# Kernel tuning notes

Hardware: AMD Instinct MI355X
Metric: run time of the kernel (lower is better)

The kernel has to match this reference:

```python
import jax, jax.numpy as jnp
import numpy as np

T, B, K = 512, 512, 128  # seq_length, batch_size, num_tags


def setup_inputs() -> dict:
    key = jax.random.key(0)
    k1, k2, k3, k4, k5 = jax.random.split(key, 5)
    emissions = jax.random.normal(k1, (T, B, K), dtype=jnp.float32)
    tags = jax.random.randint(k2, (T, B), 0, K, dtype=jnp.int32)
    mask = jnp.ones((T, B), dtype=jnp.int32)
    start_transitions = jax.random.uniform(k3, (K,), jnp.float32, -0.1, 0.1)
    end_transitions = jax.random.uniform(k4, (K,), jnp.float32, -0.1, 0.1)
    transitions = jax.random.uniform(k5, (K, K), jnp.float32, -0.1, 0.1)
    return {
        "emissions": emissions,
        "tags": tags,
        "mask": mask,
        "start_transitions": start_transitions,
        "end_transitions": end_transitions,
        "transitions": transitions,
    }


def reference(emissions, tags, mask, start_transitions, end_transitions, transitions):
    # emissions: [T,B,K], tags/mask: [T,B]; reduction='sum' (negative is the loss in practice)
    Tn, Bn, Kn = emissions.shape
    maskf = mask.astype(emissions.dtype)
    b_idx = jnp.arange(Bn)

    # ---- numerator: score of the given tag path (fully vectorized) ----
    em_tag = jnp.take_along_axis(emissions, tags[:, :, None], axis=2)[:, :, 0]  # [T,B]
    numerator = start_transitions[tags[0]] + em_tag[0]
    trans_path = transitions[tags[:-1], tags[1:]]  # [T-1,B]
    numerator = numerator + jnp.sum((trans_path + em_tag[1:]) * maskf[1:], axis=0)
    seq_ends = mask.astype(jnp.int32).sum(axis=0) - 1  # [B]
    last_tags = tags[seq_ends, b_idx]
    numerator = numerator + end_transitions[last_tags]

    # ---- denominator: forward algorithm (log-partition) via scan ----
    alpha0 = start_transitions + emissions[0]  # [B,K]

    def step(alpha, xs):
        em_i, m_i = xs  # [B,K], [B]
        # [B,K_prev,K_next] broadcast-add, logsumexp over previous tag
        nxt = jax.nn.logsumexp(alpha[:, :, None] + transitions[None, :, :] + em_i[:, None, :], axis=1)
        alpha = jnp.where(m_i[:, None], nxt, alpha)
        return alpha, None

    alpha, _ = jax.lax.scan(step, alpha0, (emissions[1:], mask[1:].astype(bool)))
    denominator = jax.nn.logsumexp(alpha + end_transitions, axis=1)  # [B]

    llh = numerator - denominator
    return jnp.sum(llh)  # reduction='sum'
```

## Files before the change

### kernel.cpp

```cpp
#include <hip/hip_runtime.h>
#include <hip/hip_bf16.h>

#define Tn 512
#define Bn 512
#define Kn 128

typedef __bf16 bf16_t;
typedef __bf16 bf16x8 __attribute__((ext_vector_type(8)));
typedef float f32x4 __attribute__((ext_vector_type(4)));
typedef unsigned int u32;
typedef u32 u32x2 __attribute__((ext_vector_type(2)));
typedef u32 u32x4 __attribute__((ext_vector_type(4)));

#define NEXPEM 4096

__device__ __forceinline__ u32 pack2bf(float a, float b) {
    bf16_t ha = (bf16_t)a, hb = (bf16_t)b;
    u32 ua = (u32)__builtin_bit_cast(unsigned short, ha);
    u32 ub = (u32)__builtin_bit_cast(unsigned short, hb);
    return ua | (ub << 16);
}

template<int PRE>
__global__ __launch_bounds__(256)
void crf_pre(const float* __restrict__ em, const int* __restrict__ tags,
             const int* __restrict__ mask, const float* __restrict__ startT,
             const float* __restrict__ endT, const float* __restrict__ trans,
             u32* __restrict__ X, bf16_t* __restrict__ frags,
             float* __restrict__ num, float* __restrict__ out)
{
    const int bid = blockIdx.x;
    const int tid = threadIdx.x;

    if (bid < NEXPEM) {
        if (!PRE) return;
        const size_t N = (size_t)Tn * Bn * Kn;
        const size_t nth = (size_t)NEXPEM * 256;
        for (size_t base = ((size_t)bid * 256 + tid) * 8; base < N; base += nth * 8) {
            const f32x4 a = *reinterpret_cast<const f32x4*>(em + base);
            const f32x4 b = *reinterpret_cast<const f32x4*>(em + base + 4);
            u32x4 w;
            w[0] = pack2bf(__expf(a[0]), __expf(a[1]));
            w[1] = pack2bf(__expf(a[2]), __expf(a[3]));
            w[2] = pack2bf(__expf(b[0]), __expf(b[1]));
            w[3] = pack2bf(__expf(b[2]), __expf(b[3]));
            *reinterpret_cast<u32x4*>(X + base / 2) = w;
        }
        return;
    }

    const int b = bid - NEXPEM;
    if (b == Bn) {
        if (tid == 0) out[0] = 0.f;
        for (int idx = tid; idx < 2*8*4*64*8; idx += blockDim.x) {
            const int e   = idx & 7;
            const int l   = (idx >> 3) & 63;
            const int ks  = (idx >> 9) & 3;
            const int m   = (idx >> 11) & 7;
            const int dir = (idx >> 14) & 1;
            const int c = l & 15, g = l >> 4;
            const int k = 32*ks + 8*g + e;
            const int j = 32*(m >> 1) + 4*(m & 1) + 8*(c >> 2) + (c & 3);
            const float v = (dir == 0) ? trans[k*Kn + j] : trans[j*Kn + k];
            frags[idx] = (bf16_t)__expf(v);
        }
        return;
    }

    float s = 0.f;
    int cnt = 0;
    for (int t = tid; t < Tn; t += 256) {
        const int mk = mask[t*Bn + b];
        cnt += (mk != 0);
        if (t >= 1 && mk != 0) {
            const int tp = tags[(t-1)*Bn + b];
            const int tc = tags[t*Bn + b];
            s += trans[tp*Kn + tc] + em[(size_t)t*Bn*Kn + (size_t)b*Kn + tc];
        }
    }
    __shared__ float sred[256];
    __shared__ int   cred[256];
    sred[tid] = s; cred[tid] = cnt;
    __syncthreads();
    for (int off = 128; off > 0; off >>= 1) {
        if (tid < off) { sred[tid] += sred[tid+off]; cred[tid] += cred[tid+off]; }
        __syncthreads();
    }
    if (tid == 0) {
        const int t0tag = tags[b];
        const float n0 = startT[t0tag] + em[(size_t)b*Kn + t0tag];
        int seq_end = cred[0] - 1;
        if (seq_end < 0) seq_end = 0;
        const int lastTag = tags[seq_end*Bn + b];
        num[b] = n0 + sred[0] + endT[lastTag];
    }
}

template<int PRE>
__global__ __launch_bounds__(512, 1)
void crf_main(const float* __restrict__ em, const u32* __restrict__ Xp,
              const int* __restrict__ maskp,
              const float* __restrict__ startT, const float* __restrict__ endT,
              const bf16_t* __restrict__ frags,
              float* __restrict__ vws, float* __restrict__ Cws)
{
    const int bid = blockIdx.x;
    const int dir = bid & 1;
    const int b0  = (bid >> 1) * 16;
    const int tid = threadIdx.x;
    const int mw  = tid >> 6;
    const int l   = tid & 63;
    const int c = l & 15, g = l >> 4;
    const int batch = b0 + c;
    const int ksw  = mw >> 1, half = mw & 1;
    const int bj   = 32*ksw + 4*half;

    __shared__ __align__(16) u32x4 exchg[2][4][64];

    bf16x8 af[4];
    {
        const bf16_t* fb = frags + (size_t)dir * 16384;
        #pragma unroll
        for (int ks = 0; ks < 4; ++ks)
            af[ks] = *reinterpret_cast<const bf16x8*>(fb + ((mw*4 + ks)*64 + l)*8);
    }

    f32x4 up;
    u32 ownprev0, ownprev1;
    float Cacc = 0.f;
    {
        const float* sv = dir ? endT : startT;
        const int t0 = dir ? 511 : 0;
        const f32x4 e4 = *reinterpret_cast<const f32x4*>(
            em + ((size_t)t0*Bn + batch)*Kn + bj + 8*g);
        const float* s4p = sv + bj + 8*g;
        f32x4 y;
        #pragma unroll
        for (int r = 0; r < 4; ++r) {
            const float s = s4p[r];
            y[r]  = __expf(s + e4[r]);
            up[r] = __expf(s);
        }
        ownprev0 = pack2bf(y[0], y[1]);
        ownprev1 = pack2bf(y[2], y[3]);
        u32* slot = reinterpret_cast<u32*>(&exchg[1][ksw][l]) + 2*half;
        u32x2 nw2 = {ownprev0, ownprev1};
        *reinterpret_cast<u32x2*>(slot) = nw2;
    }

    const int M = 256 - dir;

    const u32 laneX = (u32)(((batch*Kn) + bj + 8*g) >> 1);
    const u32 laneE = (u32)((batch*Kn) + bj + 8*g);
    const u32 laneM = (u32)batch;
    const long stepX = dir ? -(long)(Bn*Kn)   : (long)(Bn*Kn);
    const long stepE = dir ? -(long)(2*Bn*Kn) : (long)(2*Bn*Kn);
    const long stepM = dir ? -(long)(2*Bn)    : (long)(2*Bn);
    long uXA, uXB, uEA, uEB, uMA, uMB;
    {
        const int tA  = dir ? 510 : 1, tB  = dir ? 509 : 2;
        const int tmA = dir ? 511 : 1, tmB = dir ? 510 : 2;
        uXA = (long)tA * (Bn*Kn/2);  uXB = (long)tB * (Bn*Kn/2);
        uEA = (long)tA * (Bn*Kn);    uEB = (long)tB * (Bn*Kn);
        uMA = (long)tmA * Bn;        uMB = (long)tmB * Bn;
    }

    u32x2 xA, xB; f32x4 eA, eB; int mkA, mkB;
    auto load_tile = [&](u32x2& xd, f32x4& ed, int& mk, long& uX, long& uE, long& uM) {
        if (PRE) { xd = *reinterpret_cast<const u32x2*>(Xp + uX + laneX); uX += stepX; }
        else     { ed = *reinterpret_cast<const f32x4*>(em + uE + laneE); uE += stepE; }
        mk = maskp[uM + laneM]; uM += stepM;
    };

    auto iter = [&](u32x2& xcur, f32x4& ecur, int& mkcur,
                    long& uX, long& uE, long& uM, bool rs, int par) {
        asm volatile("s_waitcnt lgkmcnt(0)" ::: "memory");
        __builtin_amdgcn_s_barrier();
        __builtin_amdgcn_sched_barrier(0);

        const u32x4 bs0 = exchg[par][0][l];
        const u32x4 bs1 = exchg[par][1][l];
        const u32x4 bs2 = exchg[par][2][l];
        const u32x4 bs3 = exchg[par][3][l];

        f32x4 a0 = {0.f, 0.f, 0.f, 0.f}, a1 = {0.f, 0.f, 0.f, 0.f};
        a0 = __builtin_amdgcn_mfma_f32_16x16x32_bf16(af[0], __builtin_bit_cast(bf16x8, bs0), a0, 0, 0, 0);
        a1 = __builtin_amdgcn_mfma_f32_16x16x32_bf16(af[2], __builtin_bit_cast(bf16x8, bs2), a1, 0, 0, 0);
        a0 = __builtin_amdgcn_mfma_f32_16x16x32_bf16(af[1], __builtin_bit_cast(bf16x8, bs1), a0, 0, 0, 0);
        a1 = __builtin_amdgcn_mfma_f32_16x16x32_bf16(af[3], __builtin_bit_cast(bf16x8, bs3), a1, 0, 0, 0);
        const f32x4 acc = a0 + a1;

        const bool mk = (mkcur != 0);
        float sc = 1.f, klog = 0.f;
        if (rs) {
            int ex = (int)((bs0[0] >> 7) & 0xFF) - 127;
            ex = __shfl(ex, c, 64);
            sc = __uint_as_float((u32)((127 - ex) & 0xFF) << 23);
            klog = (float)ex * 0.6931471805599453f;
        }

        f32x4 xf;
        if (PRE) {
            xf[0] = __uint_as_float(xcur[0] << 16);
            xf[1] = __uint_as_float(xcur[0] & 0xffff0000u);
            xf[2] = __uint_as_float(xcur[1] << 16);
            xf[3] = __uint_as_float(xcur[1] & 0xffff0000u);
        } else {
            #pragma unroll
            for (int r = 0; r < 4; ++r) xf[r] = __expf(ecur[r]);
        }

        u32 nw0, nw1;
        if (dir == 0) {
            f32x4 y;
            #pragma unroll
            for (int r = 0; r < 4; ++r) {
                float a = acc[r];
                if (rs) a *= sc;
                y[r] = a * xf[r];
            }
            nw0 = pack2bf(y[0], y[1]);
            nw1 = pack2bf(y[2], y[3]);
            nw0 = mk ? nw0 : ownprev0;
            nw1 = mk ? nw1 : ownprev1;
            ownprev0 = nw0; ownprev1 = nw1;
            if (rs && mk) Cacc += klog;
        } else {
            f32x4 y;
            #pragma unroll
            for (int r = 0; r < 4; ++r) {
                float un = mk ? acc[r] : up[r];
                if (rs) un *= sc;
                up[r] = un;
                y[r] = un * xf[r];
            }
            nw0 = pack2bf(y[0], y[1]);
            nw1 = pack2bf(y[2], y[3]);
            if (rs) Cacc += klog;
        }

        u32* slot = reinterpret_cast<u32*>(&exchg[par ^ 1][ksw][l]) + 2*half;
        u32x2 nw2 = {nw0, nw1};
        *reinterpret_cast<u32x2*>(slot) = nw2;

        load_tile(xcur, ecur, mkcur, uX, uE, uM);
        __builtin_amdgcn_sched_barrier(0xF);
    };

    load_tile(xA, eA, mkA, uXA, uEA, uMA);
    load_tile(xB, eB, mkB, uXB, uEB, uMB);
    __builtin_amdgcn_sched_barrier(0xF);

    int m = 1;
    for (; m + 3 <= M; m += 4) {
        iter(xA, eA, mkA, uXA, uEA, uMA, false, 1);
        iter(xB, eB, mkB, uXB, uEB, uMB, false, 0);
        iter(xA, eA, mkA, uXA, uEA, uMA, false, 1);
        iter(xB, eB, mkB, uXB, uEB, uMB, true,  0);
    }
    for (; m <= M; ++m) {
        if (m & 1) iter(xA, eA, mkA, uXA, uEA, uMA, false, 1);
        else       iter(xB, eB, mkB, uXB, uEB, uMB, false, 0);
    }

    float* vrow = vws + ((size_t)(dir*Bn + batch))*Kn + bj + 8*g;
    f32x4 fv;
    if (dir) {
        fv = up;
    } else {
        fv[0] = __uint_as_float(ownprev0 << 16);
        fv[1] = __uint_as_float(ownprev0 & 0xffff0000u);
        fv[2] = __uint_as_float(ownprev1 << 16);
        fv[3] = __uint_as_float(ownprev1 & 0xffff0000u);
    }
    *reinterpret_cast<f32x4*>(vrow) = fv;
    if (mw == 0 && g == 0) Cws[dir*Bn + batch] = Cacc;
}

__global__ void crf_combine(const float* __restrict__ vws, const float* __restrict__ Cws,
                            const float* __restrict__ num, float* __restrict__ out)
{
    const int b = blockIdx.x;
    const int tid = threadIdx.x;
    const float p = vws[(size_t)b*Kn + tid] * vws[(size_t)(Bn + b)*Kn + tid];
    __shared__ float red[128];
    red[tid] = p;
    __syncthreads();
    for (int off = 64; off > 0; off >>= 1) {
        if (tid < off) red[tid] += red[tid + off];
        __syncthreads();
    }
    if (tid == 0) {
        const float den = Cws[b] + Cws[Bn + b] + logf(red[0]);
        atomicAdd(out, num[b] - den);
    }
}

extern "C" void kernel_launch(void* const* d_in, const int* in_sizes, int n_in,
                              void* d_out, int out_size, void* d_ws, size_t ws_size,
                              hipStream_t stream)
{
    const float* em     = (const float*)d_in[0];
    const int*   tags   = (const int*)d_in[1];
    const int*   mask   = (const int*)d_in[2];
    const float* startT = (const float*)d_in[3];
    const float* endT   = (const float*)d_in[4];
    const float* trans  = (const float*)d_in[5];

    const size_t XBYTES = (size_t)Tn * Bn * Kn * 2;
    const size_t SMALL  = 65536 + 2048 + 4096 + 524288;
    const bool pre = (ws_size >= XBYTES + SMALL);

    char* ws = (char*)d_ws;
    u32*  X  = (u32*)ws;
    char* base = pre ? (ws + XBYTES) : ws;
    bf16_t* frags = (bf16_t*)base;
    float*  num   = (float*)(base + 65536);
    float*  Cws   = (float*)(base + 65536 + 2048);
    float*  vws   = (float*)(base + 65536 + 2048 + 4096);
    float*  out   = (float*)d_out;

    if (pre) {
        hipLaunchKernelGGL((crf_pre<1>), dim3(NEXPEM + Bn + 1), dim3(256), 0, stream,
                           em, tags, mask, startT, endT, trans, X, frags, num, out);
        hipLaunchKernelGGL((crf_main<1>), dim3(64), dim3(512), 0, stream,
                           em, X, mask, startT, endT, frags, vws, Cws);
    } else {
        hipLaunchKernelGGL((crf_pre<0>), dim3(NEXPEM + Bn + 1), dim3(256), 0, stream,
                           em, tags, mask, startT, endT, trans, X, frags, num, out);
        hipLaunchKernelGGL((crf_main<0>), dim3(64), dim3(512), 0, stream,
                           em, X, mask, startT, endT, frags, vws, Cws);
    }
    hipLaunchKernelGGL(crf_combine, dim3(Bn), dim3(128), 0, stream,
                       vws, Cws, num, out);
}
```

Before: 142.9 us.

## Drop bf16 exp-emission precompute pass and compute exp inline in scan

Removes the separate pass that exponentiated the whole emission tensor into a bf16 workspace copy. The recurrent main kernel now loads fp32 emissions directly and applies exp per step. This avoids a full read-plus-write sweep over the large tensor before the scan, but doubles the bytes the latency-sensitive scan loads per step and adds exp work there. The numerator is also reworked into time-chunked per-batch partial sums that the combine kernel finishes, and the transition-fragment setup now spreads one element per thread across many blocks.

```diff
diff --git a/kernel.cpp b/kernel.cpp
--- a/kernel.cpp
+++ b/kernel.cpp
@@ -4,6 +4,7 @@
 #define Tn 512
 #define Bn 512
 #define Kn 128
+#define NUMCH 16
 
 typedef __bf16 bf16_t;
 typedef __bf16 bf16x8 __attribute__((ext_vector_type(8)));
@@ -12,8 +13,6 @@
 typedef u32 u32x2 __attribute__((ext_vector_type(2)));
 typedef u32 u32x4 __attribute__((ext_vector_type(4)));
 
-#define NEXPEM 4096
-
 __device__ __forceinline__ u32 pack2bf(float a, float b) {
     bf16_t ha = (bf16_t)a, hb = (bf16_t)b;
     u32 ua = (u32)__builtin_bit_cast(unsigned short, ha);
@@ -21,85 +20,54 @@
     return ua | (ub << 16);
 }
 
-template<int PRE>
 __global__ __launch_bounds__(256)
 void crf_pre(const float* __restrict__ em, const int* __restrict__ tags,
-             const int* __restrict__ mask, const float* __restrict__ startT,
-             const float* __restrict__ endT, const float* __restrict__ trans,
-             u32* __restrict__ X, bf16_t* __restrict__ frags,
-             float* __restrict__ num, float* __restrict__ out)
+             const int* __restrict__ mask, const float* __restrict__ trans,
+             bf16_t* __restrict__ frags, float* __restrict__ numpart,
+             int* __restrict__ cntpart, float* __restrict__ out)
 {
     const int bid = blockIdx.x;
     const int tid = threadIdx.x;
 
-    if (bid < NEXPEM) {
-        if (!PRE) return;
-        const size_t N = (size_t)Tn * Bn * Kn;
-        const size_t nth = (size_t)NEXPEM * 256;
-        for (size_t base = ((size_t)bid * 256 + tid) * 8; base < N; base += nth * 8) {
-            const f32x4 a = *reinterpret_cast<const f32x4*>(em + base);
-            const f32x4 b = *reinterpret_cast<const f32x4*>(em + base + 4);
-            u32x4 w;
-            w[0] = pack2bf(__expf(a[0]), __expf(a[1]));
-            w[1] = pack2bf(__expf(a[2]), __expf(a[3]));
-            w[2] = pack2bf(__expf(b[0]), __expf(b[1]));
-            w[3] = pack2bf(__expf(b[2]), __expf(b[3]));
-            *reinterpret_cast<u32x4*>(X + base / 2) = w;
-        }
+    if (bid < 2*NUMCH) {
+        const int ch = bid >> 1, bh = bid & 1;
+        const int b  = bh*256 + tid;
+        const int t0 = ch * (Tn / NUMCH);
+        float s = 0.f;
+        int cnt = 0;
+        int tagprev = (t0 > 0) ? tags[(t0-1)*Bn + b] : 0;
+        for (int t = t0; t < t0 + Tn/NUMCH; ++t) {
+            const int mk = mask[t*Bn + b];
+            const int tagcur = tags[t*Bn + b];
+            if (mk != 0) {
+                cnt++;
+                if (t >= 1)
+                    s += trans[tagprev*Kn + tagcur]
+                       + em[(size_t)t*Bn*Kn + (size_t)b*Kn + tagcur];
+            }
+            tagprev = tagcur;
+        }
+        numpart[ch*Bn + b] = s;
+        cntpart[ch*Bn + b] = cnt;
         return;
     }
 
-    const int b = bid - NEXPEM;
-    if (b == Bn) {
-        if (tid == 0) out[0] = 0.f;
-        for (int idx = tid; idx < 2*8*4*64*8; idx += blockDim.x) {
-            const int e   = idx & 7;
-            const int l   = (idx >> 3) & 63;
-            const int ks  = (idx >> 9) & 3;
-            const int m   = (idx >> 11) & 7;
-            const int dir = (idx >> 14) & 1;
-            const int c = l & 15, g = l >> 4;
-            const int k = 32*ks + 8*g + e;
-            const int j = 32*(m >> 1) + 4*(m & 1) + 8*(c >> 2) + (c & 3);
-            const float v = (dir == 0) ? trans[k*Kn + j] : trans[j*Kn + k];
-            frags[idx] = (bf16_t)__expf(v);
-        }
-        return;
-    }
-
-    float s = 0.f;
-    int cnt = 0;
-    for (int t = tid; t < Tn; t += 256) {
-        const int mk = mask[t*Bn + b];
-        cnt += (mk != 0);
-        if (t >= 1 && mk != 0) {
-            const int tp = tags[(t-1)*Bn + b];
-            const int tc = tags[t*Bn + b];
-            s += trans[tp*Kn + tc] + em[(size_t)t*Bn*Kn + (size_t)b*Kn + tc];
-        }
-    }
-    __shared__ float sred[256];
-    __shared__ int   cred[256];
-    sred[tid] = s; cred[tid] = cnt;
-    __syncthreads();
-    for (int off = 128; off > 0; off >>= 1) {
-        if (tid < off) { sred[tid] += sred[tid+off]; cred[tid] += cred[tid+off]; }
-        __syncthreads();
-    }
-    if (tid == 0) {
-        const int t0tag = tags[b];
-        const float n0 = startT[t0tag] + em[(size_t)b*Kn + t0tag];
-        int seq_end = cred[0] - 1;
-        if (seq_end < 0) seq_end = 0;
-        const int lastTag = tags[seq_end*Bn + b];
-        num[b] = n0 + sred[0] + endT[lastTag];
-    }
-}
-
-template<int PRE>
+    if (bid == 2*NUMCH && tid == 0) out[0] = 0.f;
+    const int idx = (bid - 2*NUMCH)*256 + tid;
+    const int e   = idx & 7;
+    const int l   = (idx >> 3) & 63;
+    const int ks  = (idx >> 9) & 3;
+    const int m   = (idx >> 11) & 7;
+    const int dir = (idx >> 14) & 1;
+    const int c = l & 15, g = l >> 4;
+    const int k = 32*ks + 8*g + e;
+    const int j = 32*(m >> 1) + 4*(m & 1) + 8*(c >> 2) + (c & 3);
+    const float v = (dir == 0) ? trans[k*Kn + j] : trans[j*Kn + k];
+    frags[idx] = (bf16_t)__expf(v);
+}
+
 __global__ __launch_bounds__(512, 1)
-void crf_main(const float* __restrict__ em, const u32* __restrict__ Xp,
-              const int* __restrict__ maskp,
+void crf_main(const float* __restrict__ em, const int* __restrict__ maskp,
               const float* __restrict__ startT, const float* __restrict__ endT,
               const bf16_t* __restrict__ frags,
               float* __restrict__ vws, float* __restrict__ Cws)
@@ -150,30 +118,25 @@
 
     const int M = 256 - dir;
 
-    const u32 laneX = (u32)(((batch*Kn) + bj + 8*g) >> 1);
     const u32 laneE = (u32)((batch*Kn) + bj + 8*g);
     const u32 laneM = (u32)batch;
-    const long stepX = dir ? -(long)(Bn*Kn)   : (long)(Bn*Kn);
     const long stepE = dir ? -(long)(2*Bn*Kn) : (long)(2*Bn*Kn);
     const long stepM = dir ? -(long)(2*Bn)    : (long)(2*Bn);
-    long uXA, uXB, uEA, uEB, uMA, uMB;
+    long uEA, uEB, uMA, uMB;
     {
         const int tA  = dir ? 510 : 1, tB  = dir ? 509 : 2;
         const int tmA = dir ? 511 : 1, tmB = dir ? 510 : 2;
-        uXA = (long)tA * (Bn*Kn/2);  uXB = (long)tB * (Bn*Kn/2);
         uEA = (long)tA * (Bn*Kn);    uEB = (long)tB * (Bn*Kn);
         uMA = (long)tmA * Bn;        uMB = (long)tmB * Bn;
     }
 
-    u32x2 xA, xB; f32x4 eA, eB; int mkA, mkB;
-    auto load_tile = [&](u32x2& xd, f32x4& ed, int& mk, long& uX, long& uE, long& uM) {
-        if (PRE) { xd = *reinterpret_cast<const u32x2*>(Xp + uX + laneX); uX += stepX; }
-        else     { ed = *reinterpret_cast<const f32x4*>(em + uE + laneE); uE += stepE; }
+    f32x4 eA, eB; int mkA, mkB;
+    auto load_tile = [&](f32x4& ed, int& mk, long& uE, long& uM) {
+        ed = *reinterpret_cast<const f32x4*>(em + uE + laneE); uE += stepE;
         mk = maskp[uM + laneM]; uM += stepM;
     };
 
-    auto iter = [&](u32x2& xcur, f32x4& ecur, int& mkcur,
-                    long& uX, long& uE, long& uM, bool rs, int par) {
+    auto iter = [&](f32x4& ecur, int& mkcur, long& uE, long& uM, bool rs, int par) {
         asm volatile("s_waitcnt lgkmcnt(0)" ::: "memory");
         __builtin_amdgcn_s_barrier();
         __builtin_amdgcn_sched_barrier(0);
@@ -200,15 +163,8 @@
         }
 
         f32x4 xf;
-        if (PRE) {
-            xf[0] = __uint_as_float(xcur[0] << 16);
-            xf[1] = __uint_as_float(xcur[0] & 0xffff0000u);
-            xf[2] = __uint_as_float(xcur[1] << 16);
-            xf[3] = __uint_as_float(xcur[1] & 0xffff0000u);
-        } else {
-            #pragma unroll
-            for (int r = 0; r < 4; ++r) xf[r] = __expf(ecur[r]);
-        }
+        #pragma unroll
+        for (int r = 0; r < 4; ++r) xf[r] = __expf(ecur[r]);
 
         u32 nw0, nw1;
         if (dir == 0) {
@@ -243,24 +199,24 @@
         u32x2 nw2 = {nw0, nw1};
         *reinterpret_cast<u32x2*>(slot) = nw2;
 
-        load_tile(xcur, ecur, mkcur, uX, uE, uM);
+        load_tile(ecur, mkcur, uE, uM);
         __builtin_amdgcn_sched_barrier(0xF);
     };
 
-    load_tile(xA, eA, mkA, uXA, uEA, uMA);
-    load_tile(xB, eB, mkB, uXB, uEB, uMB);
+    load_tile(eA, mkA, uEA, uMA);
+    load_tile(eB, mkB, uEB, uMB);
     __builtin_amdgcn_sched_barrier(0xF);
 
     int m = 1;
     for (; m + 3 <= M; m += 4) {
-        iter(xA, eA, mkA, uXA, uEA, uMA, false, 1);
-        iter(xB, eB, mkB, uXB, uEB, uMB, false, 0);
-        iter(xA, eA, mkA, uXA, uEA, uMA, false, 1);
-        iter(xB, eB, mkB, uXB, uEB, uMB, true,  0);
+        iter(eA, mkA, uEA, uMA, false, 1);
+        iter(eB, mkB, uEB, uMB, false, 0);
+        iter(eA, mkA, uEA, uMA, false, 1);
+        iter(eB, mkB, uEB, uMB, true,  0);
     }
     for (; m <= M; ++m) {
-        if (m & 1) iter(xA, eA, mkA, uXA, uEA, uMA, false, 1);
-        else       iter(xB, eB, mkB, uXB, uEB, uMB, false, 0);
+        if (m & 1) iter(eA, mkA, uEA, uMA, false, 1);
+        else       iter(eB, mkB, uEB, uMB, false, 0);
     }
 
     float* vrow = vws + ((size_t)(dir*Bn + batch))*Kn + bj + 8*g;
@@ -278,21 +234,35 @@
 }
 
 __global__ void crf_combine(const float* __restrict__ vws, const float* __restrict__ Cws,
-                            const float* __restrict__ num, float* __restrict__ out)
+                            const float* __restrict__ numpart, const int* __restrict__ cntpart,
+                            const int* __restrict__ tags, const float* __restrict__ em,
+                            const float* __restrict__ startT, const float* __restrict__ endT,
+                            float* __restrict__ out)
 {
     const int b = blockIdx.x;
     const int tid = threadIdx.x;
     const float p = vws[(size_t)b*Kn + tid] * vws[(size_t)(Bn + b)*Kn + tid];
     __shared__ float red[128];
+    __shared__ float sp[NUMCH];
+    __shared__ int   cp[NUMCH];
     red[tid] = p;
+    if (tid < NUMCH) { sp[tid] = numpart[tid*Bn + b]; cp[tid] = cntpart[tid*Bn + b]; }
     __syncthreads();
     for (int off = 64; off > 0; off >>= 1) {
         if (tid < off) red[tid] += red[tid + off];
         __syncthreads();
     }
     if (tid == 0) {
+        float s = 0.f; int cnt = 0;
+        #pragma unroll
+        for (int ch = 0; ch < NUMCH; ++ch) { s += sp[ch]; cnt += cp[ch]; }
+        const int t0tag = tags[b];
+        int seq_end = cnt - 1;
+        if (seq_end < 0) seq_end = 0;
+        const int lastTag = tags[seq_end*Bn + b];
+        const float num = startT[t0tag] + em[(size_t)b*Kn + t0tag] + s + endT[lastTag];
         const float den = Cws[b] + Cws[Bn + b] + logf(red[0]);
-        atomicAdd(out, num[b] - den);
+        atomicAdd(out, num - den);
     }
 }
 
@@ -307,30 +277,18 @@
     const float* endT   = (const float*)d_in[4];
     const float* trans  = (const float*)d_in[5];
 
-    const size_t XBYTES = (size_t)Tn * Bn * Kn * 2;
-    const size_t SMALL  = 65536 + 2048 + 4096 + 524288;
-    const bool pre = (ws_size >= XBYTES + SMALL);
-
     char* ws = (char*)d_ws;
-    u32*  X  = (u32*)ws;
-    char* base = pre ? (ws + XBYTES) : ws;
-    bf16_t* frags = (bf16_t*)base;
-    float*  num   = (float*)(base + 65536);
-    float*  Cws   = (float*)(base + 65536 + 2048);
-    float*  vws   = (float*)(base + 65536 + 2048 + 4096);
-    float*  out   = (float*)d_out;
-
-    if (pre) {
-        hipLaunchKernelGGL((crf_pre<1>), dim3(NEXPEM + Bn + 1), dim3(256), 0, stream,
-                           em, tags, mask, startT, endT, trans, X, frags, num, out);
-        hipLaunchKernelGGL((crf_main<1>), dim3(64), dim3(512), 0, stream,
-                           em, X, mask, startT, endT, frags, vws, Cws);
-    } else {
-        hipLaunchKernelGGL((crf_pre<0>), dim3(NEXPEM + Bn + 1), dim3(256), 0, stream,
-                           em, tags, mask, startT, endT, trans, X, frags, num, out);
-        hipLaunchKernelGGL((crf_main<0>), dim3(64), dim3(512), 0, stream,
-                           em, X, mask, startT, endT, frags, vws, Cws);
-    }
+    bf16_t* frags   = (bf16_t*)ws;
+    float*  Cws     = (float*)(ws + 65536);
+    float*  vws     = (float*)(ws + 69632);
+    float*  numpart = (float*)(ws + 593920);
+    int*    cntpart = (int*)(ws + 626688);
+    float*  out     = (float*)d_out;
+
+    hipLaunchKernelGGL(crf_pre, dim3(2*NUMCH + 128), dim3(256), 0, stream,
+                       em, tags, mask, trans, frags, numpart, cntpart, out);
+    hipLaunchKernelGGL(crf_main, dim3(64), dim3(512), 0, stream,
+                       em, mask, startT, endT, frags, vws, Cws);
     hipLaunchKernelGGL(crf_combine, dim3(Bn), dim3(128), 0, stream,
-                       vws, Cws, num, out);
-}
+                       vws, Cws, numpart, cntpart, tags, em, startT, endT, out);
+}
```

New measurement: 124.8 us. 1.15x faster.

## Restructure numerator into coalesced per-batch time chunks and spread frag build across blocks

Applied to the files above, without the earlier changes.

The numerator path-score pass changes from one block per batch element, which strides over time with uncoalesced loads, to 32 blocks where each thread owns one batch element and walks a chunk of time steps. Tag and mask loads become coalesced across threads. Partial sums and counts go to the workspace, and the final start, end and chunk reduction moves into the combine kernel. The transition-fragment exp table is now spread over 128 blocks instead of one block looping over 16K elements. The intent is to shorten the preprocessing kernel's tail and cut its block count. In exchange, the gathered emission loads are still scattered, and only 32 blocks now do that work.

```diff
diff --git a/kernel.cpp b/kernel.cpp
--- a/kernel.cpp
+++ b/kernel.cpp
@@ -4,6 +4,8 @@
 #define Tn 512
 #define Bn 512
 #define Kn 128
+#define NUMCH 16
+#define NEXPEM 4096
 
 typedef __bf16 bf16_t;
 typedef __bf16 bf16x8 __attribute__((ext_vector_type(8)));
@@ -12,8 +14,6 @@
 typedef u32 u32x2 __attribute__((ext_vector_type(2)));
 typedef u32 u32x4 __attribute__((ext_vector_type(4)));
 
-#define NEXPEM 4096
-
 __device__ __forceinline__ u32 pack2bf(float a, float b) {
     bf16_t ha = (bf16_t)a, hb = (bf16_t)b;
     u32 ua = (u32)__builtin_bit_cast(unsigned short, ha);
@@ -24,10 +24,10 @@
 template<int PRE>
 __global__ __launch_bounds__(256)
 void crf_pre(const float* __restrict__ em, const int* __restrict__ tags,
-             const int* __restrict__ mask, const float* __restrict__ startT,
-             const float* __restrict__ endT, const float* __restrict__ trans,
+             const int* __restrict__ mask, const float* __restrict__ trans,
              u32* __restrict__ X, bf16_t* __restrict__ frags,
-             float* __restrict__ num, float* __restrict__ out)
+             float* __restrict__ numpart, int* __restrict__ cntpart,
+             float* __restrict__ out)
 {
     const int bid = blockIdx.x;
     const int tid = threadIdx.x;
@@ -49,51 +49,42 @@
         return;
     }
 
-    const int b = bid - NEXPEM;
-    if (b == Bn) {
-        if (tid == 0) out[0] = 0.f;
-        for (int idx = tid; idx < 2*8*4*64*8; idx += blockDim.x) {
-            const int e   = idx & 7;
-            const int l   = (idx >> 3) & 63;
-            const int ks  = (idx >> 9) & 3;
-            const int m   = (idx >> 11) & 7;
-            const int dir = (idx >> 14) & 1;
-            const int c = l & 15, g = l >> 4;
-            const int k = 32*ks + 8*g + e;
-            const int j = 32*(m >> 1) + 4*(m & 1) + 8*(c >> 2) + (c & 3);
-            const float v = (dir == 0) ? trans[k*Kn + j] : trans[j*Kn + k];
-            frags[idx] = (bf16_t)__expf(v);
-        }
+    const int b2 = bid - NEXPEM;
+    if (b2 < 2*NUMCH) {
+        const int ch = b2 >> 1, bh = b2 & 1;
+        const int b  = bh*256 + tid;
+        const int t0 = ch * (Tn / NUMCH);
+        float s = 0.f;
+        int cnt = 0;
+        int tagprev = (t0 > 0) ? tags[(t0-1)*Bn + b] : 0;
+        for (int t = t0; t < t0 + Tn/NUMCH; ++t) {
+            const int mk = mask[t*Bn + b];
+            const int tagcur = tags[t*Bn + b];
+            if (mk != 0) {
+                cnt++;
+                if (t >= 1)
+                    s += trans[tagprev*Kn + tagcur]
+                       + em[(size_t)t*Bn*Kn + (size_t)b*Kn + tagcur];
+            }
+            tagprev = tagcur;
+        }
+        numpart[ch*Bn + b] = s;
+        cntpart[ch*Bn + b] = cnt;
         return;
     }
 
-    float s = 0.f;
-    int cnt = 0;
-    for (int t = tid; t < Tn; t += 256) {
-        const int mk = mask[t*Bn + b];
-        cnt += (mk != 0);
-        if (t >= 1 && mk != 0) {
-            const int tp = tags[(t-1)*Bn + b];
-            const int tc = tags[t*Bn + b];
-            s += trans[tp*Kn + tc] + em[(size_t)t*Bn*Kn + (size_t)b*Kn + tc];
-        }
-    }
-    __shared__ float sred[256];
-    __shared__ int   cred[256];
-    sred[tid] = s; cred[tid] = cnt;
-    __syncthreads();
-    for (int off = 128; off > 0; off >>= 1) {
-        if (tid < off) { sred[tid] += sred[tid+off]; cred[tid] += cred[tid+off]; }
-        __syncthreads();
-    }
-    if (tid == 0) {
-        const int t0tag = tags[b];
-        const float n0 = startT[t0tag] + em[(size_t)b*Kn + t0tag];
-        int seq_end = cred[0] - 1;
-        if (seq_end < 0) seq_end = 0;
-        const int lastTag = tags[seq_end*Bn + b];
-        num[b] = n0 + sred[0] + endT[lastTag];
-    }
+    if (b2 == 2*NUMCH && tid == 0) out[0] = 0.f;
+    const int idx = (b2 - 2*NUMCH)*256 + tid;
+    const int e   = idx & 7;
+    const int l   = (idx >> 3) & 63;
+    const int ks  = (idx >> 9) & 3;
+    const int m   = (idx >> 11) & 7;
+    const int dir = (idx >> 14) & 1;
+    const int c = l & 15, g = l >> 4;
+    const int k = 32*ks + 8*g + e;
+    const int j = 32*(m >> 1) + 4*(m & 1) + 8*(c >> 2) + (c & 3);
+    const float v = (dir == 0) ? trans[k*Kn + j] : trans[j*Kn + k];
+    frags[idx] = (bf16_t)__expf(v);
 }
 
 template<int PRE>
@@ -278,21 +269,35 @@
 }
 
 __global__ void crf_combine(const float* __restrict__ vws, const float* __restrict__ Cws,
-                            const float* __restrict__ num, float* __restrict__ out)
+                            const float* __restrict__ numpart, const int* __restrict__ cntpart,
+                            const int* __restrict__ tags, const float* __restrict__ em,
+                            const float* __restrict__ startT, const float* __restrict__ endT,
+                            float* __restrict__ out)
 {
     const int b = blockIdx.x;
     const int tid = threadIdx.x;
     const float p = vws[(size_t)b*Kn + tid] * vws[(size_t)(Bn + b)*Kn + tid];
     __shared__ float red[128];
+    __shared__ float sp[NUMCH];
+    __shared__ int   cp[NUMCH];
     red[tid] = p;
+    if (tid < NUMCH) { sp[tid] = numpart[tid*Bn + b]; cp[tid] = cntpart[tid*Bn + b]; }
     __syncthreads();
     for (int off = 64; off > 0; off >>= 1) {
         if (tid < off) red[tid] += red[tid + off];
         __syncthreads();
     }
     if (tid == 0) {
+        float s = 0.f; int cnt = 0;
+        #pragma unroll
+        for (int ch = 0; ch < NUMCH; ++ch) { s += sp[ch]; cnt += cp[ch]; }
+        const int t0tag = tags[b];
+        int seq_end = cnt - 1;
+        if (seq_end < 0) seq_end = 0;
+        const int lastTag = tags[seq_end*Bn + b];
+        const float num = startT[t0tag] + em[(size_t)b*Kn + t0tag] + s + endT[lastTag];
         const float den = Cws[b] + Cws[Bn + b] + logf(red[0]);
-        atomicAdd(out, num[b] - den);
+        atomicAdd(out, num - den);
     }
 }
 
@@ -308,29 +313,30 @@
     const float* trans  = (const float*)d_in[5];
 
     const size_t XBYTES = (size_t)Tn * Bn * Kn * 2;
-    const size_t SMALL  = 65536 + 2048 + 4096 + 524288;
+    const size_t SMALL  = 65536 + 4096 + 524288 + 32768 + 32768;
     const bool pre = (ws_size >= XBYTES + SMALL);
 
     char* ws = (char*)d_ws;
     u32*  X  = (u32*)ws;
     char* base = pre ? (ws + XBYTES) : ws;
-    bf16_t* frags = (bf16_t*)base;
-    float*  num   = (float*)(base + 65536);
-    float*  Cws   = (float*)(base + 65536 + 2048);
-    float*  vws   = (float*)(base + 65536 + 2048 + 4096);
-    float*  out   = (float*)d_out;
+    bf16_t* frags   = (bf16_t*)base;
+    float*  Cws     = (float*)(base + 65536);
+    float*  vws     = (float*)(base + 69632);
+    float*  numpart = (float*)(base + 593920);
+    int*    cntpart = (int*)(base + 626688);
+    float*  out     = (float*)d_out;
 
     if (pre) {
-        hipLaunchKernelGGL((crf_pre<1>), dim3(NEXPEM + Bn + 1), dim3(256), 0, stream,
-                           em, tags, mask, startT, endT, trans, X, frags, num, out);
+        hipLaunchKernelGGL((crf_pre<1>), dim3(NEXPEM + 2*NUMCH + 128), dim3(256), 0, stream,
+                           em, tags, mask, trans, X, frags, numpart, cntpart, out);
         hipLaunchKernelGGL((crf_main<1>), dim3(64), dim3(512), 0, stream,
                            em, X, mask, startT, endT, frags, vws, Cws);
     } else {
-        hipLaunchKernelGGL((crf_pre<0>), dim3(NEXPEM + Bn + 1), dim3(256), 0, stream,
-                           em, tags, mask, startT, endT, trans, X, frags, num, out);
+        hipLaunchKernelGGL((crf_pre<0>), dim3(NEXPEM + 2*NUMCH + 128), dim3(256), 0, stream,
+                           em, tags, mask, trans, X, frags, numpart, cntpart, out);
         hipLaunchKernelGGL((crf_main<0>), dim3(64), dim3(512), 0, stream,
                            em, X, mask, startT, endT, frags, vws, Cws);
     }
     hipLaunchKernelGGL(crf_combine, dim3(Bn), dim3(128), 0, stream,
-                       vws, Cws, num, out);
-}
+                       vws, Cws, numpart, cntpart, tags, em, startT, endT, out);
+}
```

Measured after the change: 142.2 us. About the same (-0.5%).
